# Kernel tuning notes

Measured on AMD Instinct MI355X. Metric: run time of the kernel, lower is better.

Reference implementation:

```python
import jax, jax.numpy as jnp
import numpy as np

B = 128      # batch
HW = 224     # image height/width
P = 16       # patch size
D = 512      # token_dim
NH = 8       # n_heads
L = 6        # t_blocks
M = 2048     # mlp_layer_size
NC = 10      # output classes
GP = HW // P            # patches per side
T = GP * GP + 1         # tokens incl. class token (197)
EPS = 1e-5


def _ln(x, g, b):
    m = jnp.mean(x, axis=-1, keepdims=True)
    v = jnp.mean(jnp.square(x - m), axis=-1, keepdims=True)
    return (x - m) / jnp.sqrt(v + EPS) * g + b


def setup_inputs() -> dict:
    key = jax.random.key(0)
    ks = iter(jax.random.split(key, 32))
    s = 0.02
    inp = {
        "images": jax.random.normal(next(ks), (B, 1, HW, HW), dtype=jnp.float32),
        "lin_map_w": jax.random.normal(next(ks), (D, P * P), dtype=jnp.float32) * s,
        "lin_map_b": jnp.zeros((D,), jnp.float32),
        "class_token": jax.random.uniform(next(ks), (1, D), dtype=jnp.float32),
        "ln1_g": jnp.ones((L, D), jnp.float32),
        "ln1_b": jnp.zeros((L, D), jnp.float32),
        "ln2_g": jnp.ones((L, D), jnp.float32),
        "ln2_b": jnp.zeros((L, D), jnp.float32),
        "qw": jax.random.normal(next(ks), (L, NH, D, D), dtype=jnp.float32) * s,
        "qb": jnp.zeros((L, NH, D), jnp.float32),
        "kw": jax.random.normal(next(ks), (L, NH, D, D), dtype=jnp.float32) * s,
        "kb": jnp.zeros((L, NH, D), jnp.float32),
        "vw": jax.random.normal(next(ks), (L, NH, D, D), dtype=jnp.float32) * s,
        "vb": jnp.zeros((L, NH, D), jnp.float32),
        "map_w": jax.random.normal(next(ks), (L, T, T * NH), dtype=jnp.float32) * s,
        "map_b": jnp.zeros((L, T), jnp.float32),
        "mlp_w1": jax.random.normal(next(ks), (L, M, D), dtype=jnp.float32) * s,
        "mlp_b1": jnp.zeros((L, M), jnp.float32),
        "mlp_w2": jax.random.normal(next(ks), (L, D, M), dtype=jnp.float32) * s,
        "mlp_b2": jnp.zeros((L, D), jnp.float32),
        "cls_w": jax.random.normal(next(ks), (NC, D), dtype=jnp.float32) * s,
        "cls_b": jnp.zeros((NC,), jnp.float32),
    }
    return inp


def reference(images, lin_map_w, lin_map_b, class_token, ln1_g, ln1_b, ln2_g, ln2_b,
              qw, qb, kw, kb, vw, vb, map_w, map_b,
              mlp_w1, mlp_b1, mlp_w2, mlp_b2, cls_w, cls_b):
    n = images.shape[0]
    img = images[:, 0]  # (B, HW, HW), channel squeezed as in patching_func
    # non-overlapping patch extraction (patchify with step=patch_size)
    patches = img.reshape(n, GP, P, GP, P).transpose(0, 1, 3, 2, 4).reshape(n, GP * GP, P * P)
    emb = patches @ lin_map_w.T + lin_map_b                 # (B, nP, D)
    cls = jnp.broadcast_to(class_token, (n, 1, D))
    x = jnp.concatenate([cls, emb], axis=1)                 # (B, T, D)
    scale = 1.0 / np.sqrt(T - 1)                            # quirky scale from source
    for l in range(L):
        h = _ln(x, ln1_g[l], ln1_b[l])
        q = jnp.einsum('btd,hed->bhte', h, qw[l]) + qb[l][None, :, None, :]
        k = jnp.einsum('btd,hed->bhte', h, kw[l]) + kb[l][None, :, None, :]
        v = jnp.einsum('btd,hed->bhte', h, vw[l]) + vb[l][None, :, None, :]
        attn = jax.nn.softmax(jnp.einsum('bhte,bhse->bhts', q, k) * scale, axis=-1)
        av = jnp.einsum('bhts,bhse->bhte', attn, v)         # (B, NH, T, D)
        res = av.reshape(n, NH * T, D)                      # head-major concat along tokens
        msa = jnp.einsum('bmd,tm->btd', res, map_w[l]) + map_b[l][None, :, None]
        x = x + msa
        y = _ln(x, ln2_g[l], ln2_b[l])
        mlp = jax.nn.gelu(y @ mlp_w1[l].T + mlp_b1[l], approximate=False) @ mlp_w2[l].T + mlp_b2[l]
        x = y + mlp                                         # note: residual uses ln2(x), per source
    logits = x[:, 0] @ cls_w.T + cls_b
    return jax.nn.softmax(logits, axis=-1)
```

## Files before the change

kernel.cpp:

```cpp
#include <hip/hip_runtime.h>
#include <hip/hip_bf16.h>
#include <math.h>

#define B_   128
#define HW_  224
#define P_   16
#define D_   512
#define NH_  8
#define L_   6
#define M_   2048
#define NC_  10
#define GP_  14
#define T_   197
#define TP_  224
#define EPS_ 1e-5f
#define ZVW2_ 2048
#define RCW_ 448

typedef __hip_bfloat16 bf16;
typedef __attribute__((ext_vector_type(8))) __bf16 bf16x8;
typedef __attribute__((ext_vector_type(4))) float  f32x4;

__device__ __forceinline__ void gload16(const void* g, void* l) {
    __builtin_amdgcn_global_load_lds(
        (const __attribute__((address_space(1))) void*)g,
        (__attribute__((address_space(3))) void*)l, 16, 0, 0);
}


__global__ void k_f32_to_bf16v(const float* __restrict__ in, bf16* __restrict__ out, long n8) {
    long stride = (long)gridDim.x * blockDim.x;
    for (long i = (long)blockIdx.x * blockDim.x + threadIdx.x; i < n8; i += stride) {
        float4 a = ((const float4*)in)[i * 2], b = ((const float4*)in)[i * 2 + 1];
        union { uint4 u; bf16 h[8]; } r;
        r.h[0] = __float2bfloat16(a.x); r.h[1] = __float2bfloat16(a.y);
        r.h[2] = __float2bfloat16(a.z); r.h[3] = __float2bfloat16(a.w);
        r.h[4] = __float2bfloat16(b.x); r.h[5] = __float2bfloat16(b.y);
        r.h[6] = __float2bfloat16(b.z); r.h[7] = __float2bfloat16(b.w);
        ((uint4*)out)[i] = r.u;
    }
}

__global__ void k_f32_to_bf16v2(const float* __restrict__ in1, bf16* __restrict__ out1,
                                const float* __restrict__ in2, bf16* __restrict__ out2, long n8) {
    long stride = (long)gridDim.x * blockDim.x;
    for (long i = (long)blockIdx.x * blockDim.x + threadIdx.x; i < n8; i += stride) {
        {
            float4 a = ((const float4*)in1)[i * 2], b = ((const float4*)in1)[i * 2 + 1];
            union { uint4 u; bf16 h[8]; } r;
            r.h[0] = __float2bfloat16(a.x); r.h[1] = __float2bfloat16(a.y);
            r.h[2] = __float2bfloat16(a.z); r.h[3] = __float2bfloat16(a.w);
            r.h[4] = __float2bfloat16(b.x); r.h[5] = __float2bfloat16(b.y);
            r.h[6] = __float2bfloat16(b.z); r.h[7] = __float2bfloat16(b.w);
            ((uint4*)out1)[i] = r.u;
        }
        {
            float4 a = ((const float4*)in2)[i * 2], b = ((const float4*)in2)[i * 2 + 1];
            union { uint4 u; bf16 h[8]; } r;
            r.h[0] = __float2bfloat16(a.x); r.h[1] = __float2bfloat16(a.y);
            r.h[2] = __float2bfloat16(a.z); r.h[3] = __float2bfloat16(a.w);
            r.h[4] = __float2bfloat16(b.x); r.h[5] = __float2bfloat16(b.y);
            r.h[6] = __float2bfloat16(b.z); r.h[7] = __float2bfloat16(b.w);
            ((uint4*)out2)[i] = r.u;
        }
    }
}

__global__ void k_prep_wv(const float* __restrict__ vw, bf16* __restrict__ wzv) {
    int idx = blockIdx.x * blockDim.x + threadIdx.x;
    if (idx >= NH_ * D_ * (D_ / 8)) return;
    int d8 = idx & 63;
    int e  = (idx >> 6) & 511;
    int h  = idx >> 15;
    long so = ((long)(h * D_ + e)) * D_ + d8 * 8;
    float4 a = *(const float4*)(vw + so), b = *(const float4*)(vw + so + 4);
    union { uint4 u; bf16 hh[8]; } rr;
    rr.hh[0] = __float2bfloat16(a.x); rr.hh[1] = __float2bfloat16(a.y);
    rr.hh[2] = __float2bfloat16(a.z); rr.hh[3] = __float2bfloat16(a.w);
    rr.hh[4] = __float2bfloat16(b.x); rr.hh[5] = __float2bfloat16(b.y);
    rr.hh[6] = __float2bfloat16(b.z); rr.hh[7] = __float2bfloat16(b.w);
    ((uint4*)wzv)[((long)(h * 1024 + 512 + e)) * 64 + d8] = rr.u;
}

__global__ void k_prep_ub(const float* __restrict__ kw, const float* __restrict__ qb,
                          const float* __restrict__ vb, float* __restrict__ out) {
    int idx = blockIdx.x * blockDim.x + threadIdx.x;
    if (idx >= NH_ * 1024) return;
    int j = idx & 1023, h = idx >> 10;
    if (j < 512) {
        const float* kwh = kw + (long)h * D_ * D_ + j;
        const float* qbh = qb + h * D_;
        float s = 0.f;
        for (int e = 0; e < D_; e++) s += kwh[(long)e * D_] * qbh[e];
        out[idx] = s;
    } else {
        out[idx] = vb[h * D_ + (j - 512)];
    }
}

__global__ void k_patchify(const float* __restrict__ img, bf16* __restrict__ patches) {
    long idx = (long)blockIdx.x * blockDim.x + threadIdx.x;
    long total = (long)B_ * 196 * 256;
    if (idx >= total) return;
    int q = (int)(idx & 255);
    int p = (int)((idx >> 8) % 196);
    int b = (int)(idx / (196 * 256));
    int gy = p / GP_, gx = p % GP_;
    int py = q >> 4,  px = q & 15;
    patches[idx] = __float2bfloat16(img[((long)b * HW_ + gy * P_ + py) * HW_ + gx * P_ + px]);
}

__global__ void k_cls_token(const float* __restrict__ tok, float* __restrict__ x) {
    int i = blockIdx.x * blockDim.x + threadIdx.x;
    if (i < B_ * D_) {
        int b = i >> 9, d = i & 511;
        x[(long)b * T_ * D_ + d] = tok[d];
    }
}

__global__ void k_prep_map(const float* __restrict__ in, bf16* __restrict__ out) {
    int idx = blockIdx.x * blockDim.x + threadIdx.x;
    int total = NH_ * T_ * TP_;
    if (idx >= total) return;
    int s = idx % TP_;
    int t = (idx / TP_) % T_;
    int h = idx / (TP_ * T_);
    float v = (s < T_) ? in[t * (T_ * NH_) + h * T_ + s] : 0.f;
    out[idx] = __float2bfloat16(v);
}


template<int WRITE_Y>
__global__ __launch_bounds__(256) void k_ln(const float* x,
        const float* __restrict__ g, const float* __restrict__ bb,
        bf16* __restrict__ obf, float* of, int rows) {
    int wid = blockIdx.x * 4 + (threadIdx.x >> 6);
    if (wid >= rows) return;
    int lane = threadIdx.x & 63;
    const float* xr = x + (long)wid * D_;
    float v[8];
    float s = 0.f;
#pragma unroll
    for (int i = 0; i < 8; i++) { v[i] = xr[i * 64 + lane]; s += v[i]; }
#pragma unroll
    for (int off = 32; off; off >>= 1) s += __shfl_xor(s, off, 64);
    float mean = s * (1.f / D_);
    float sq = 0.f;
#pragma unroll
    for (int i = 0; i < 8; i++) { float d = v[i] - mean; sq += d * d; }
#pragma unroll
    for (int off = 32; off; off >>= 1) sq += __shfl_xor(sq, off, 64);
    float inv = rsqrtf(sq * (1.f / D_) + EPS_);
#pragma unroll
    for (int i = 0; i < 8; i++) {
        int d = i * 64 + lane;
        float val = (v[i] - mean) * inv * g[d] + bb[d];
        obf[(long)wid * D_ + d] = __float2bfloat16(val);
        if (WRITE_Y) of[(long)wid * D_ + d] = val;
    }
}


__global__ __launch_bounds__(256) void k_attn_ssm2(
        const bf16* __restrict__ Qbase, long ldq, long qImg, long qHead,
        const bf16* __restrict__ Kbase, long ldk, long kImg,
        bf16* __restrict__ Pm, float scale) {
    __shared__ __align__(16) bf16 Qs[128][32];
    __shared__ __align__(16) bf16 Ks[256][32];
    int z = blockIdx.z;
    int img = z & 127, h2 = z >> 7;
    int q0 = blockIdx.y * 128;
    int tid = threadIdx.x;
    int wv = tid >> 6, lane = tid & 63;

    const bf16* Qp = Qbase + (long)img * qImg + (long)h2 * qHead;
    const bf16* Kp = Kbase + (long)img * kImg;

    int sRow = 16 * wv + (lane >> 2);
    int sCol = (lane & 3) * 8;
    const bf16* gQ = Qp + (long)(q0 + sRow) * ldq + sCol;
    const bf16* gK = Kp + (long)sRow * ldk + sCol;
    char* lQ = (char*)Qs + (16 * wv) * 64;
    char* lK = (char*)Ks + (16 * wv) * 64;

    f32x4 acc[2][13];
#pragma unroll
    for (int j = 0; j < 2; j++)
#pragma unroll
        for (int f = 0; f < 13; f++) acc[j][f] = (f32x4){0.f, 0.f, 0.f, 0.f};

    for (int kt = 0; kt < 16; kt++) {
        long k0 = (long)kt * 32;
        gload16(gQ + k0, lQ);
        gload16(gQ + 64 * ldq + k0, lQ + 4096);
#pragma unroll
        for (int p = 0; p < 4; p++)
            gload16(gK + (long)(p * 64) * ldk + k0, lK + p * 4096);
        __syncthreads();
        bf16x8 af[2];
#pragma unroll
        for (int j = 0; j < 2; j++)
            af[j] = *(const bf16x8*)&Qs[wv * 32 + j * 16 + (lane & 15)][(lane >> 4) * 8];
#pragma unroll
        for (int f = 0; f < 13; f++) {
            bf16x8 bfr = *(const bf16x8*)&Ks[f * 16 + (lane & 15)][(lane >> 4) * 8];
            acc[0][f] = __builtin_amdgcn_mfma_f32_16x16x32_bf16(af[0], bfr, acc[0][f], 0, 0, 0);
            acc[1][f] = __builtin_amdgcn_mfma_f32_16x16x32_bf16(af[1], bfr, acc[1][f], 0, 0, 0);
        }
        __syncthreads();
    }

    int c1 = lane & 15, grp = lane >> 4;
    const bf16 z0 = __float2bfloat16(0.f);
#pragma unroll
    for (int j = 0; j < 2; j++) {
        float mx[4] = {-1e30f, -1e30f, -1e30f, -1e30f};
        float sm[4] = {0.f, 0.f, 0.f, 0.f};
#pragma unroll
        for (int f = 0; f < 13; f++) {
            bool val = (f * 16 + c1 < T_);
#pragma unroll
            for (int r = 0; r < 4; r++) {
                float v = val ? acc[j][f][r] * scale : -1e30f;
                acc[j][f][r] = v;
                mx[r] = fmaxf(mx[r], v);
            }
        }
#pragma unroll
        for (int r = 0; r < 4; r++)
#pragma unroll
            for (int off = 1; off < 16; off <<= 1) mx[r] = fmaxf(mx[r], __shfl_xor(mx[r], off, 64));
#pragma unroll
        for (int f = 0; f < 13; f++) {
            bool val = (f * 16 + c1 < T_);
#pragma unroll
            for (int r = 0; r < 4; r++) {
                float e = val ? expf(acc[j][f][r] - mx[r]) : 0.f;
                acc[j][f][r] = e;
                sm[r] += e;
            }
        }
#pragma unroll
        for (int r = 0; r < 4; r++) {
#pragma unroll
            for (int off = 1; off < 16; off <<= 1) sm[r] += __shfl_xor(sm[r], off, 64);
            sm[r] = 1.f / sm[r];
        }
#pragma unroll
        for (int r = 0; r < 4; r++) {
            int qi = q0 + wv * 32 + j * 16 + grp * 4 + r;
            if (qi >= T_) continue;
            bf16* prow = Pm + ((long)z * T_ + qi) * TP_;
#pragma unroll
            for (int f = 0; f < 13; f++)
                prow[f * 16 + c1] = __float2bfloat16(acc[j][f][r] * sm[r]);
            prow[208 + c1] = z0;
        }
    }
}


__device__ __forceinline__ float geluf(float v) {
    return 0.5f * v * (1.f + erff(v * 0.70710678118654752f));
}

template<int MODE, bool GUARD>
__global__ __launch_bounds__(256) void k_gemm_bt(
        const bf16* __restrict__ A, long lda, long bsA,
        const bf16* __restrict__ Bw, long ldb, long bsB,
        void* __restrict__ Cp, long ldc, long bsC,
        const float* __restrict__ bias,
        const float* res, long ldres,
        int Mt, int Nt, int Kt) {
    __shared__ __align__(16) bf16 As[128][32];
    __shared__ __align__(16) bf16 Bs[128][32];
    int bz = blockIdx.z;
    A  += (long)bz * bsA;
    Bw += (long)bz * bsB;
    int m0 = blockIdx.y * 128, n0 = blockIdx.x * 128;
    int tid = threadIdx.x;
    int wv = tid >> 6, lane = tid & 63;
    int wm = (wv >> 1) * 64, wn = (wv & 1) * 64;
    int lrow = lane & 15, koff = (lane >> 4) * 8;

    int rA = tid >> 2, pA = (tid & 3) * 8;
    const bf16* gA0 = A  + (long)(m0 + rA) * lda + pA;
    const bf16* gA1 = A  + (long)(m0 + 64 + rA) * lda + pA;
    const bf16* gB0 = Bw + (long)(n0 + rA) * ldb + pA;
    const bf16* gB1 = Bw + (long)(n0 + 64 + rA) * ldb + pA;
    char* lA0 = (char*)As + (wv * 64) * 16;
    char* lA1 = (char*)As + (256 + wv * 64) * 16;
    char* lB0 = (char*)Bs + (wv * 64) * 16;
    char* lB1 = (char*)Bs + (256 + wv * 64) * 16;

    f32x4 acc[4][4];
#pragma unroll
    for (int i = 0; i < 4; i++)
#pragma unroll
        for (int j = 0; j < 4; j++) acc[i][j] = (f32x4){0.f, 0.f, 0.f, 0.f};

    int kTiles = Kt >> 5;
    for (int kt = 0; kt < kTiles; kt++) {
        long k0 = (long)kt << 5;
        gload16(gA0 + k0, lA0);
        gload16(gA1 + k0, lA1);
        gload16(gB0 + k0, lB0);
        gload16(gB1 + k0, lB1);
        __syncthreads();
        bf16x8 af[4], bfr[4];
#pragma unroll
        for (int mi = 0; mi < 4; mi++) af[mi]  = *(const bf16x8*)&As[wm + mi * 16 + lrow][koff];
#pragma unroll
        for (int ni = 0; ni < 4; ni++) bfr[ni] = *(const bf16x8*)&Bs[wn + ni * 16 + lrow][koff];
#pragma unroll
        for (int mi = 0; mi < 4; mi++)
#pragma unroll
            for (int ni = 0; ni < 4; ni++)
                acc[mi][ni] = __builtin_amdgcn_mfma_f32_16x16x32_bf16(af[mi], bfr[ni], acc[mi][ni], 0, 0, 0);
        __syncthreads();
    }

    int r4 = (lane >> 4) * 4, c1 = lane & 15;
    float bv[4];
#pragma unroll
    for (int ni = 0; ni < 4; ni++) {
        int col = n0 + wn + ni * 16 + c1;
        bv[ni] = (bias && (!GUARD || col < Nt)) ? bias[col] : 0.f;
    }
#pragma unroll
    for (int mi = 0; mi < 4; mi++) {
#pragma unroll
        for (int r = 0; r < 4; r++) {
            int row = m0 + wm + mi * 16 + r4 + r;
            if (GUARD && row >= Mt) continue;
            long base = (long)bz * bsC + (long)row * ldc + n0 + wn + c1;
#pragma unroll
            for (int ni = 0; ni < 4; ni++) {
                if (GUARD && (n0 + wn + ni * 16 + c1) >= Nt) continue;
                float v = acc[mi][ni][r] + bv[ni];
                long cidx = base + ni * 16;
                if (MODE == 0)      ((float*)Cp)[cidx] = v;
                else if (MODE == 1) ((bf16*)Cp)[cidx]  = __float2bfloat16(v);
                else if (MODE == 2) ((bf16*)Cp)[cidx]  = __float2bfloat16(geluf(v));
                else                ((float*)Cp)[cidx] = v + res[(long)row * ldres + n0 + wn + c1 + ni * 16];
            }
        }
    }
}

__global__ __launch_bounds__(256) void k_gemm_r(
        const bf16* __restrict__ mapPair,
        const bf16* __restrict__ Pb,
        bf16* __restrict__ Rcat) {
    __shared__ __align__(16) bf16 As[128][32];
    __shared__ __align__(16) bf16 Bs[128][32];
    int z = blockIdx.z;
    int img = z & 127, h2 = z >> 7;
    const bf16* A  = mapPair + (long)h2 * T_ * TP_;
    const bf16* Bw = Pb + ((long)(h2 * 128 + img)) * (long)T_ * TP_;
    bf16* Cp = Rcat + (long)img * 224 * RCW_ + h2 * 224;
    int m0 = blockIdx.y * 128, n0 = blockIdx.x * 128;
    int tid = threadIdx.x;
    int wv = tid >> 6, lane = tid & 63;
    int wm = (wv >> 1) * 64, wn = (wv & 1) * 64;
    int lrow = lane & 15, koff = (lane >> 4) * 8;

    int rA = tid >> 2, pA = (tid & 3) * 8;
    const bf16* gA0 = A + (long)(m0 + rA) * TP_ + pA;
    const bf16* gA1 = A + (long)(m0 + 64 + rA) * TP_ + pA;
    char* lA0 = (char*)As + (wv * 64) * 16;
    char* lA1 = (char*)As + (256 + wv * 64) * 16;
    int bk = tid & 31, bg = tid >> 5;

    f32x4 acc[4][4];
#pragma unroll
    for (int i = 0; i < 4; i++)
#pragma unroll
        for (int j = 0; j < 4; j++) acc[i][j] = (f32x4){0.f, 0.f, 0.f, 0.f};

    for (int kt = 0; kt < 7; kt++) {
        long k0 = (long)kt << 5;
        gload16(gA0 + k0, lA0);
        gload16(gA1 + k0, lA1);
#pragma unroll
        for (int i = 0; i < 2; i++) {
            int g = bg + 8 * i;
            uint4 v = *(const uint4*)(Bw + (k0 + bk) * TP_ + n0 + g * 8);
            const bf16* pv = (const bf16*)&v;
#pragma unroll
            for (int j = 0; j < 8; j++) Bs[g * 8 + j][bk] = pv[j];
        }
        __syncthreads();
        bf16x8 af[4], bfr[4];
#pragma unroll
        for (int mi = 0; mi < 4; mi++) af[mi]  = *(const bf16x8*)&As[wm + mi * 16 + lrow][koff];
#pragma unroll
        for (int ni = 0; ni < 4; ni++) bfr[ni] = *(const bf16x8*)&Bs[wn + ni * 16 + lrow][koff];
#pragma unroll
        for (int mi = 0; mi < 4; mi++)
#pragma unroll
            for (int ni = 0; ni < 4; ni++)
                acc[mi][ni] = __builtin_amdgcn_mfma_f32_16x16x32_bf16(af[mi], bfr[ni], acc[mi][ni], 0, 0, 0);
        __syncthreads();
    }

    int r4 = (lane >> 4) * 4, c1 = lane & 15;
#pragma unroll
    for (int mi = 0; mi < 4; mi++) {
#pragma unroll
        for (int r = 0; r < 4; r++) {
            int row = m0 + wm + mi * 16 + r4 + r;
            if (row >= T_) continue;
#pragma unroll
            for (int ni = 0; ni < 4; ni++) {
                int col = n0 + wn + ni * 16 + c1;
                if (col >= 224) continue;
                Cp[(long)row * RCW_ + col] = __float2bfloat16(acc[mi][ni][r]);
            }
        }
    }
}

__global__ __launch_bounds__(256) void k_gemm_rv(
        const bf16* __restrict__ Rcat,
        const bf16* __restrict__ ZV,
        float* __restrict__ xf,
        const float* __restrict__ rowbias) {
    __shared__ __align__(16) bf16 As[128][32];
    __shared__ __align__(16) bf16 Bs[128][32];
    int img = blockIdx.z;
    const bf16* A = Rcat + (long)img * 224 * RCW_;
    const bf16* Vimg = ZV + (long)img * T_ * ZVW2_;
    float* Cp = xf + (long)img * T_ * D_;
    int m0 = blockIdx.y * 128, n0 = blockIdx.x * 128;
    int tid = threadIdx.x;
    int wv = tid >> 6, lane = tid & 63;
    int wm = (wv >> 1) * 64, wn = (wv & 1) * 64;
    int lrow = lane & 15, koff = (lane >> 4) * 8;

    int rA = tid >> 2, pA = (tid & 3) * 8;
    const bf16* gA0 = A + (long)(m0 + rA) * RCW_ + pA;
    const bf16* gA1 = A + (long)(m0 + 64 + rA) * RCW_ + pA;
    char* lA0 = (char*)As + (wv * 64) * 16;
    char* lA1 = (char*)As + (256 + wv * 64) * 16;
    int bk = tid & 31, bg = tid >> 5;

    f32x4 acc[4][4];
#pragma unroll
    for (int i = 0; i < 4; i++)
#pragma unroll
        for (int j = 0; j < 4; j++) acc[i][j] = (f32x4){0.f, 0.f, 0.f, 0.f};

    for (int kt = 0; kt < 14; kt++) {
        long k0 = (long)kt << 5;
        gload16(gA0 + k0, lA0);
        gload16(gA1 + k0, lA1);
        const bf16* Vb = (kt < 7) ? (Vimg + 512 + k0 * ZVW2_)
                                  : (Vimg + 1536 + (k0 - 224) * ZVW2_);
#pragma unroll
        for (int i = 0; i < 2; i++) {
            int g = bg + 8 * i;
            uint4 v = *(const uint4*)(Vb + (long)bk * ZVW2_ + n0 + g * 8);
            const bf16* pv = (const bf16*)&v;
#pragma unroll
            for (int j = 0; j < 8; j++) Bs[g * 8 + j][bk] = pv[j];
        }
        __syncthreads();
        bf16x8 af[4], bfr[4];
#pragma unroll
        for (int mi = 0; mi < 4; mi++) af[mi]  = *(const bf16x8*)&As[wm + mi * 16 + lrow][koff];
#pragma unroll
        for (int ni = 0; ni < 4; ni++) bfr[ni] = *(const bf16x8*)&Bs[wn + ni * 16 + lrow][koff];
#pragma unroll
        for (int mi = 0; mi < 4; mi++)
#pragma unroll
            for (int ni = 0; ni < 4; ni++)
                acc[mi][ni] = __builtin_amdgcn_mfma_f32_16x16x32_bf16(af[mi], bfr[ni], acc[mi][ni], 0, 0, 0);
        __syncthreads();
    }

    int r4 = (lane >> 4) * 4, c1 = lane & 15;
#pragma unroll
    for (int mi = 0; mi < 4; mi++) {
#pragma unroll
        for (int r = 0; r < 4; r++) {
            int row = m0 + wm + mi * 16 + r4 + r;
            if (row >= T_) continue;
            float rb = rowbias ? rowbias[row] : 0.f;
#pragma unroll
            for (int ni = 0; ni < 4; ni++) {
                int col = n0 + wn + ni * 16 + c1;
                Cp[(long)row * D_ + col] += acc[mi][ni][r] + rb * 0.25f;
            }
        }
    }
}

__global__ __launch_bounds__(256) void k_gemm_tn(
        const bf16* __restrict__ A, long lda, long bsA,
        const bf16* __restrict__ Bw, long ldb, long bsB,
        bf16* __restrict__ Cp, long ldc, long bsC,
        int Mt, int Nt, int Kt) {
    __shared__ __align__(16) bf16 As[128][32];
    __shared__ __align__(16) bf16 Bs[128][32];
    int bz = blockIdx.z;
    A  += (long)bz * bsA;
    Bw += (long)bz * bsB;
    int m0 = blockIdx.y * 128, n0 = blockIdx.x * 128;
    int tid = threadIdx.x;
    int wv = tid >> 6, lane = tid & 63;
    int wm = (wv >> 1) * 64, wn = (wv & 1) * 64;
    int lrow = lane & 15, koff = (lane >> 4) * 8;
    int bk = tid & 31, bg = tid >> 5;

    f32x4 acc[4][4];
#pragma unroll
    for (int i = 0; i < 4; i++)
#pragma unroll
        for (int j = 0; j < 4; j++) acc[i][j] = (f32x4){0.f, 0.f, 0.f, 0.f};

    int kTiles = Kt >> 5;
    for (int kt = 0; kt < kTiles; kt++) {
        long k0 = (long)kt << 5;
#pragma unroll
        for (int i = 0; i < 2; i++) {
            int g = bg + 8 * i;
            uint4 va = *(const uint4*)(A + (k0 + bk) * lda + m0 + g * 8);
            const bf16* pa = (const bf16*)&va;
#pragma unroll
            for (int j = 0; j < 8; j++) As[g * 8 + j][bk] = pa[j];
            uint4 vb = *(const uint4*)(Bw + (k0 + bk) * ldb + n0 + g * 8);
            const bf16* pb = (const bf16*)&vb;
#pragma unroll
            for (int j = 0; j < 8; j++) Bs[g * 8 + j][bk] = pb[j];
        }
        __syncthreads();
        bf16x8 af[4], bfr[4];
#pragma unroll
        for (int mi = 0; mi < 4; mi++) af[mi]  = *(const bf16x8*)&As[wm + mi * 16 + lrow][koff];
#pragma unroll
        for (int ni = 0; ni < 4; ni++) bfr[ni] = *(const bf16x8*)&Bs[wn + ni * 16 + lrow][koff];
#pragma unroll
        for (int mi = 0; mi < 4; mi++)
#pragma unroll
            for (int ni = 0; ni < 4; ni++)
                acc[mi][ni] = __builtin_amdgcn_mfma_f32_16x16x32_bf16(af[mi], bfr[ni], acc[mi][ni], 0, 0, 0);
        __syncthreads();
    }

    int r4 = (lane >> 4) * 4, c1 = lane & 15;
#pragma unroll
    for (int mi = 0; mi < 4; mi++) {
#pragma unroll
        for (int r = 0; r < 4; r++) {
            int row = m0 + wm + mi * 16 + r4 + r;
            if (row >= Mt) continue;
#pragma unroll
            for (int ni = 0; ni < 4; ni++) {
                int col = n0 + wn + ni * 16 + c1;
                if (col >= Nt) continue;
                Cp[(long)bz * bsC + (long)row * ldc + col] = __float2bfloat16(acc[mi][ni][r]);
            }
        }
    }
}


__global__ __launch_bounds__(64) void k_classifier(const float* __restrict__ x,
        const float* __restrict__ w, const float* __restrict__ bias, float* __restrict__ out) {
    int b = blockIdx.x, lane = threadIdx.x;
    const float* xr = x + (long)b * T_ * D_;
    float logits[NC_];
#pragma unroll
    for (int c = 0; c < NC_; c++) {
        float s = 0.f;
        for (int d = lane; d < D_; d += 64) s += xr[d] * w[c * D_ + d];
#pragma unroll
        for (int off = 32; off; off >>= 1) s += __shfl_xor(s, off, 64);
        logits[c] = s + bias[c];
    }
    float mx = -1e30f;
#pragma unroll
    for (int c = 0; c < NC_; c++) mx = fmaxf(mx, logits[c]);
    float sum = 0.f;
#pragma unroll
    for (int c = 0; c < NC_; c++) { float e = expf(logits[c] - mx); logits[c] = e; sum += e; }
    if (lane == 0) {
        float inv = 1.f / sum;
#pragma unroll
        for (int c = 0; c < NC_; c++) out[(long)b * NC_ + c] = logits[c] * inv;
    }
}


extern "C" void kernel_launch(void* const* d_in, const int* in_sizes, int n_in,
                              void* d_out, int out_size, void* d_ws, size_t ws_size,
                              hipStream_t stream) {
    const float* images  = (const float*)d_in[0];
    const float* lin_w   = (const float*)d_in[1];
    const float* lin_b   = (const float*)d_in[2];
    const float* cls_tok = (const float*)d_in[3];
    const float* ln1_g   = (const float*)d_in[4];
    const float* ln1_b   = (const float*)d_in[5];
    const float* ln2_g   = (const float*)d_in[6];
    const float* ln2_b   = (const float*)d_in[7];
    const float* qw      = (const float*)d_in[8];
    const float* qb      = (const float*)d_in[9];
    const float* kw      = (const float*)d_in[10];
    const float* kb      = (const float*)d_in[11];
    const float* vw      = (const float*)d_in[12];
    const float* vb      = (const float*)d_in[13];
    const float* map_w   = (const float*)d_in[14];
    const float* map_b   = (const float*)d_in[15];
    const float* w1      = (const float*)d_in[16];
    const float* b1      = (const float*)d_in[17];
    const float* w2      = (const float*)d_in[18];
    const float* b2      = (const float*)d_in[19];
    const float* cls_w   = (const float*)d_in[20];
    const float* cls_b   = (const float*)d_in[21];

    char* wp = (char*)d_ws;
    auto alloc = [&](size_t bytes) { char* p = wp; wp += (bytes + 255) & ~(size_t)255; return p; };
    const long BT = (long)B_ * T_;

    float* xf   = (float*)alloc(BT * D_ * 4);
    bf16*  hb   = (bf16*) alloc((BT + 192) * D_ * 2);
    bf16*  ZVh2 = (bf16*) alloc((size_t)(BT + 160) * ZVW2_ * 2);
    bf16*  m1c  = ZVh2;
    bf16*  Pb2  = (bf16*) alloc(((size_t)256 * T_ + 64) * TP_ * 2);
    char*  rcReg= alloc(((size_t)128 * 224 + 64) * RCW_ * 2);
    bf16*  Rcat = (bf16*)rcReg;
    bf16*  patches = (bf16*)rcReg;
    bf16*  wqb  = (bf16*)rcReg;
    bf16*  wkb  = (bf16*)(rcReg + (long)NH_ * D_ * D_ * 2);
    bf16*  wzv  = (bf16*) alloc(((long)NH_ * 1024 + 64) * D_ * 2);
    float* zvb  = (float*)alloc((long)NH_ * 1024 * 4);
    bf16*  wmapP= (bf16*) alloc(((long)NH_ * T_ + 64) * TP_ * 2);
    bf16*  w1l  = (bf16*) alloc((long)(M_ + 64) * D_ * 2);
    bf16*  w2l  = (bf16*) alloc((long)(D_ + 64) * M_ * 2);
    bf16*  wlin = (bf16*) alloc((long)(D_ + 64) * 256 * 2);

    k_f32_to_bf16v<<<1024, 256, 0, stream>>>(lin_w, wlin, (long)D_ * 256 / 8);
    {
        long tot = (long)B_ * 196 * 256;
        k_patchify<<<(int)((tot + 255) / 256), 256, 0, stream>>>(images, patches);
        k_cls_token<<<(B_ * D_ + 255) / 256, 256, 0, stream>>>(cls_tok, xf);
        k_gemm_bt<0, true><<<dim3(4, 2, B_), 256, 0, stream>>>(
            patches, 256, (long)196 * 256,
            wlin, 256, 0,
            xf + D_, D_, (long)T_ * D_,
            lin_b, nullptr, 0,
            196, D_, 256);
    }

    const float scale = 1.0f / 14.0f;
    const int lnGrid = (int)((BT + 3) / 4);

    for (int l = 0; l < L_; l++) {
        k_f32_to_bf16v2<<<1024, 256, 0, stream>>>(
            qw + (long)l * NH_ * D_ * D_, wqb,
            kw + (long)l * NH_ * D_ * D_, wkb, (long)NH_ * D_ * D_ / 8);
        k_gemm_tn<<<dim3(4, 4, NH_), 256, 0, stream>>>(
            wkb, D_, (long)D_ * D_,
            wqb, D_, (long)D_ * D_,
            wzv, D_, (long)1024 * D_,
            D_, D_, D_);
        k_prep_wv<<<(NH_ * D_ * (D_ / 8) + 255) / 256, 256, 0, stream>>>(
            vw + (long)l * NH_ * D_ * D_, wzv);
        k_prep_ub<<<(NH_ * 1024 + 255) / 256, 256, 0, stream>>>(
            kw + (long)l * NH_ * D_ * D_, qb + (long)l * NH_ * D_,
            vb + (long)l * NH_ * D_, zvb);
        k_f32_to_bf16v2<<<1024, 256, 0, stream>>>(
            w1 + (long)l * M_ * D_, w1l,
            w2 + (long)l * D_ * M_, w2l, (long)M_ * D_ / 8);
        k_prep_map<<<(NH_ * T_ * TP_ + 255) / 256, 256, 0, stream>>>(
            map_w + (long)l * T_ * T_ * NH_, wmapP);

        k_ln<0><<<lnGrid, 256, 0, stream>>>(xf, ln1_g + l * D_, ln1_b + l * D_, hb, nullptr, (int)BT);

        for (int hp = 0; hp < 4; hp++) {
            k_gemm_bt<1, false><<<dim3(16, 197, 1), 256, 0, stream>>>(
                hb, D_, 0, wzv + (long)hp * 2048 * D_, D_, 0,
                ZVh2, ZVW2_, 0, zvb + (long)hp * 2048, nullptr, 0,
                (int)BT, ZVW2_, D_);

            k_attn_ssm2<<<dim3(1, 2, 256), 256, 0, stream>>>(
                ZVh2, ZVW2_, (long)T_ * ZVW2_, 1024,
                hb, D_, (long)T_ * D_,
                Pb2, scale);

            k_gemm_r<<<dim3(2, 2, 256), 256, 0, stream>>>(
                wmapP + (long)(hp * 2) * T_ * TP_, Pb2, Rcat);

            k_gemm_rv<<<dim3(4, 2, B_), 256, 0, stream>>>(
                Rcat, ZVh2, xf, map_b + (long)l * T_);
        }

        k_ln<1><<<lnGrid, 256, 0, stream>>>(xf, ln2_g + l * D_, ln2_b + l * D_, hb, xf, (int)BT);

        k_gemm_bt<2, false><<<dim3(16, 197, 1), 256, 0, stream>>>(
            hb, D_, 0, w1l, D_, 0,
            m1c, M_, 0, b1 + (long)l * M_, nullptr, 0, (int)BT, M_, D_);
        k_gemm_bt<3, false><<<dim3(4, 197, 1), 256, 0, stream>>>(
            m1c, M_, 0, w2l, M_, 0,
            xf, D_, 0, b2 + (long)l * D_, xf, D_, (int)BT, D_, M_);
    }

    k_classifier<<<B_, 64, 0, stream>>>(xf, cls_w, cls_b, (float*)d_out);
}
```

Baseline: 7.860 ms.

## Double-buffer LDS tiles in GEMM and attention-score kernels to overlap loads

Both the generic bt-GEMM kernel and the attention score kernel now use two LDS buffers. Each iteration reads the current tile's fragments into registers, then issues the direct-to-LDS global loads for the next k-tile before running the MFMAs. This hides global-memory latency behind compute and removes one of the two barriers per k-step. The cost is doubled LDS use, which can lower occupancy. The last iteration also prefetches one tile past the end of K, which may read out of bounds.

Result: slower. 8.089 ms (+2.9%).

```diff
diff --git a/kernel.cpp b/kernel.cpp
--- a/kernel.cpp
+++ b/kernel.cpp
@@ -27,6 +27,11 @@
         (__attribute__((address_space(3))) void*)l, 16, 0, 0);
 }
 
+#define SCHED0_ __builtin_amdgcn_sched_barrier(0)
+#define VMCNT0_BARRIER_ do { \
+    asm volatile("s_waitcnt vmcnt(0)" ::: "memory"); \
+    SCHED0_; __builtin_amdgcn_s_barrier(); SCHED0_; } while (0)
+
 
 __global__ void k_f32_to_bf16v(const float* __restrict__ in, bf16* __restrict__ out, long n8) {
     long stride = (long)gridDim.x * blockDim.x;
@@ -165,8 +170,8 @@
         const bf16* __restrict__ Qbase, long ldq, long qImg, long qHead,
         const bf16* __restrict__ Kbase, long ldk, long kImg,
         bf16* __restrict__ Pm, float scale) {
-    __shared__ __align__(16) bf16 Qs[128][32];
-    __shared__ __align__(16) bf16 Ks[256][32];
+    __shared__ __align__(16) bf16 Qs[2][128][32];
+    __shared__ __align__(16) bf16 Ks[2][256][32];
     int z = blockIdx.z;
     int img = z & 127, h2 = z >> 7;
     int q0 = blockIdx.y * 128;
@@ -180,8 +185,17 @@
     int sCol = (lane & 3) * 8;
     const bf16* gQ = Qp + (long)(q0 + sRow) * ldq + sCol;
     const bf16* gK = Kp + (long)sRow * ldk + sCol;
-    char* lQ = (char*)Qs + (16 * wv) * 64;
-    char* lK = (char*)Ks + (16 * wv) * 64;
+    char* lQw = (char*)Qs + (16 * wv) * 64;
+    char* lKw = (char*)Ks + (16 * wv) * 64;
+
+    auto stage = [&](int buf, int kt) {
+        long k0 = (long)kt * 32;
+        gload16(gQ + k0, lQw + buf * 8192);
+        gload16(gQ + 64 * ldq + k0, lQw + buf * 8192 + 4096);
+#pragma unroll
+        for (int p = 0; p < 4; p++)
+            gload16(gK + (long)(p * 64) * ldk + k0, lKw + buf * 16384 + p * 4096);
+    };
 
     f32x4 acc[2][13];
 #pragma unroll
@@ -189,25 +203,28 @@
 #pragma unroll
         for (int f = 0; f < 13; f++) acc[j][f] = (f32x4){0.f, 0.f, 0.f, 0.f};
 
+    stage(0, 0);
+    VMCNT0_BARRIER_;
+    int cur = 0;
     for (int kt = 0; kt < 16; kt++) {
-        long k0 = (long)kt * 32;
-        gload16(gQ + k0, lQ);
-        gload16(gQ + 64 * ldq + k0, lQ + 4096);
-#pragma unroll
-        for (int p = 0; p < 4; p++)
-            gload16(gK + (long)(p * 64) * ldk + k0, lK + p * 4096);
-        __syncthreads();
         bf16x8 af[2];
 #pragma unroll
         for (int j = 0; j < 2; j++)
-            af[j] = *(const bf16x8*)&Qs[wv * 32 + j * 16 + (lane & 15)][(lane >> 4) * 8];
+            af[j] = *(const bf16x8*)&Qs[cur][wv * 32 + j * 16 + (lane & 15)][(lane >> 4) * 8];
+        bf16x8 bfr[13];
+#pragma unroll
+        for (int f = 0; f < 13; f++)
+            bfr[f] = *(const bf16x8*)&Ks[cur][f * 16 + (lane & 15)][(lane >> 4) * 8];
+        SCHED0_;
+        stage(cur ^ 1, kt + 1);
+        SCHED0_;
 #pragma unroll
         for (int f = 0; f < 13; f++) {
-            bf16x8 bfr = *(const bf16x8*)&Ks[f * 16 + (lane & 15)][(lane >> 4) * 8];
-            acc[0][f] = __builtin_amdgcn_mfma_f32_16x16x32_bf16(af[0], bfr, acc[0][f], 0, 0, 0);
-            acc[1][f] = __builtin_amdgcn_mfma_f32_16x16x32_bf16(af[1], bfr, acc[1][f], 0, 0, 0);
-        }
-        __syncthreads();
+            acc[0][f] = __builtin_amdgcn_mfma_f32_16x16x32_bf16(af[0], bfr[f], acc[0][f], 0, 0, 0);
+            acc[1][f] = __builtin_amdgcn_mfma_f32_16x16x32_bf16(af[1], bfr[f], acc[1][f], 0, 0, 0);
+        }
+        VMCNT0_BARRIER_;
+        cur ^= 1;
     }
 
     int c1 = lane & 15, grp = lane >> 4;
@@ -272,8 +289,8 @@
         const float* __restrict__ bias,
         const float* res, long ldres,
         int Mt, int Nt, int Kt) {
-    __shared__ __align__(16) bf16 As[128][32];
-    __shared__ __align__(16) bf16 Bs[128][32];
+    __shared__ __align__(16) bf16 As[2][128][32];
+    __shared__ __align__(16) bf16 Bs[2][128][32];
     int bz = blockIdx.z;
     A  += (long)bz * bsA;
     Bw += (long)bz * bsB;
@@ -293,6 +310,14 @@
     char* lB0 = (char*)Bs + (wv * 64) * 16;
     char* lB1 = (char*)Bs + (256 + wv * 64) * 16;
 
+    auto stage = [&](int buf, int kt) {
+        long k0 = (long)kt << 5;
+        gload16(gA0 + k0, lA0 + buf * 8192);
+        gload16(gA1 + k0, lA1 + buf * 8192);
+        gload16(gB0 + k0, lB0 + buf * 8192);
+        gload16(gB1 + k0, lB1 + buf * 8192);
+    };
+
     f32x4 acc[4][4];
 #pragma unroll
     for (int i = 0; i < 4; i++)
@@ -300,24 +325,25 @@
         for (int j = 0; j < 4; j++) acc[i][j] = (f32x4){0.f, 0.f, 0.f, 0.f};
 
     int kTiles = Kt >> 5;
+    stage(0, 0);
+    VMCNT0_BARRIER_;
+    int cur = 0;
     for (int kt = 0; kt < kTiles; kt++) {
-        long k0 = (long)kt << 5;
-        gload16(gA0 + k0, lA0);
-        gload16(gA1 + k0, lA1);
-        gload16(gB0 + k0, lB0);
-        gload16(gB1 + k0, lB1);
-        __syncthreads();
         bf16x8 af[4], bfr[4];
 #pragma unroll
-        for (int mi = 0; mi < 4; mi++) af[mi]  = *(const bf16x8*)&As[wm + mi * 16 + lrow][koff];
-#pragma unroll
-        for (int ni = 0; ni < 4; ni++) bfr[ni] = *(const bf16x8*)&Bs[wn + ni * 16 + lrow][koff];
+        for (int mi = 0; mi < 4; mi++) af[mi]  = *(const bf16x8*)&As[cur][wm + mi * 16 + lrow][koff];
+#pragma unroll
+        for (int ni = 0; ni < 4; ni++) bfr[ni] = *(const bf16x8*)&Bs[cur][wn + ni * 16 + lrow][koff];
+        SCHED0_;
+        stage(cur ^ 1, kt + 1);
+        SCHED0_;
 #pragma unroll
         for (int mi = 0; mi < 4; mi++)
 #pragma unroll
             for (int ni = 0; ni < 4; ni++)
                 acc[mi][ni] = __builtin_amdgcn_mfma_f32_16x16x32_bf16(af[mi], bfr[ni], acc[mi][ni], 0, 0, 0);
-        __syncthreads();
+        VMCNT0_BARRIER_;
+        cur ^= 1;
     }
 
     int r4 = (lane >> 4) * 4, c1 = lane & 15;
```
